# Kernel tuning notes

Measured on AMD Instinct MI355X. Metric: run time of the kernel, lower is better.

The kernel has to match this reference:

```python
import jax, jax.numpy as jnp
import numpy as np

N = 100000
E = 1600000
IN_CH = 128
HID = 32
HEADS = 4
OUT_CH = 32
NEG_SLOPE = 0.2


def _gat_layer(x, W, a_src, a_dst, b, src, dst, heads, out_ch):
    """PyG-style GATConv (concat=True). x: [N, F_in]; returns [N, heads*out_ch]."""
    n = x.shape[0]
    h = (x @ W).reshape(n, heads, out_ch)                    # [N, H, C]
    alpha_s = jnp.einsum('nhc,hc->nh', h, a_src)             # [N, H]
    alpha_d = jnp.einsum('nhc,hc->nh', h, a_dst)             # [N, H]
    logits = jax.nn.leaky_relu(alpha_s[src] + alpha_d[dst], NEG_SLOPE)  # [E, H]
    # segment softmax over destination node
    m = jax.ops.segment_max(logits, dst, num_segments=n)
    m = jnp.where(jnp.isfinite(m), m, 0.0)
    p = jnp.exp(logits - m[dst])
    denom = jax.ops.segment_sum(p, dst, num_segments=n)
    alpha = p / (denom[dst] + 1e-16)                         # [E, H]
    msg = h[src] * alpha[..., None]                          # [E, H, C]
    out = jax.ops.segment_sum(msg, dst, num_segments=n)      # [N, H, C]
    return out.reshape(n, heads * out_ch) + b


def setup_inputs() -> dict:
    key = jax.random.key(0)
    ks = jax.random.split(key, 16)
    x = jax.random.normal(ks[0], (N, IN_CH), dtype=jnp.float32)
    edge_index = jax.random.randint(ks[1], (2, E), 0, N, dtype=jnp.int32)

    def glorot(k, shape):
        fan = shape[0] + shape[-1]
        return jax.random.normal(k, shape, dtype=jnp.float32) * np.sqrt(2.0 / fan)

    hid = HID * HEADS  # 128
    return {
        'x': x,
        'edge_index': edge_index,
        'W1': glorot(ks[2], (IN_CH, hid)),
        'a_src1': glorot(ks[3], (HEADS, HID)),
        'a_dst1': glorot(ks[4], (HEADS, HID)),
        'b1': jnp.zeros((hid,), jnp.float32),
        'W2': glorot(ks[5], (hid, hid)),
        'a_src2': glorot(ks[6], (HEADS, HID)),
        'a_dst2': glorot(ks[7], (HEADS, HID)),
        'b2': jnp.zeros((hid,), jnp.float32),
        'W3': glorot(ks[8], (hid, OUT_CH)),
        'a_src3': glorot(ks[9], (1, OUT_CH)),
        'a_dst3': glorot(ks[10], (1, OUT_CH)),
        'b3': jnp.zeros((OUT_CH,), jnp.float32),
    }


def reference(x, edge_index, W1, a_src1, a_dst1, b1, W2, a_src2, a_dst2, b2,
              W3, a_src3, a_dst3, b3):
    # add self-loops (PyG GATConv default add_self_loops=True)
    loop = jnp.arange(N, dtype=edge_index.dtype)
    src = jnp.concatenate([edge_index[0], loop])
    dst = jnp.concatenate([edge_index[1], loop])

    h = _gat_layer(x, W1, a_src1, a_dst1, b1, src, dst, HEADS, HID)
    h = jax.nn.elu(h)
    h = _gat_layer(h, W2, a_src2, a_dst2, b2, src, dst, HEADS, HID)
    h = jax.nn.elu(h)
    out = _gat_layer(h, W3, a_src3, a_dst3, b3, src, dst, 1, OUT_CH)
    return out
```

## Files before the change

kernel.cpp:

```cpp
#include <hip/hip_runtime.h>
#include <cstdint>

#define NN 100000
#define EE 1600000
#define ET (EE + NN)
#define NBUCK 782
#define BCAP 3584
#define G_GEMM 1563
#define G_FILL 256
#define G_WPREP 80

typedef unsigned int u32;
typedef unsigned short u16;
typedef short bf16x8 __attribute__((ext_vector_type(8)));
typedef float f32x4 __attribute__((ext_vector_type(4)));

__device__ __forceinline__ u16 f2bf(float f) {
    union { float f; u32 i; } v; v.f = f;
    u32 r = v.i + 0x7FFFu + ((v.i >> 16) & 1u);
    return (u16)(r >> 16);
}
__device__ __forceinline__ float bf_lo(u32 u) {
    union { u32 i; float f; } v; v.i = u << 16; return v.f;
}
__device__ __forceinline__ float bf_hi(u32 u) {
    union { u32 i; float f; } v; v.i = u & 0xffff0000u; return v.f;
}
__device__ __forceinline__ void get_edge(const int* __restrict__ ei, int e, int& s, int& d) {
    if (e < EE) { s = ei[e]; d = ei[EE + e]; }
    else { s = e - EE; d = s; }
}
__device__ __forceinline__ float leaky(float x) { return x > 0.f ? x : 0.2f * x; }

template<int OUTC, bool IN16, bool WCVT>
__device__ __forceinline__ void gemm_body(int r0, u32* lds,
    const void* __restrict__ Xv, const void* __restrict__ Wsrc,
    const float* __restrict__ asw, const float* __restrict__ adw,
    u16* __restrict__ Hout16, float* __restrict__ as_o, float* __restrict__ ad_o, int tid)
{
    constexpr int NT = OUTC / 16;
    constexpr int HS = (OUTC == 128) ? 132 : 36;
    u32* wl = lds + 64 * 68;

    if (IN16) {
        const u32* Xg = (const u32*)Xv;
        for (int i = tid; i < 64 * 64; i += 256) {
            int r = i >> 6, k2 = i & 63;
            u32 v = 0;
            if (r0 + r < NN) v = Xg[(size_t)(r0 + r) * 64 + k2];
            lds[r * 68 + k2] = v;
        }
    } else {
        const float* Xf = (const float*)Xv;
        for (int i = tid; i < 64 * 64; i += 256) {
            int r = i >> 6, k2 = i & 63;
            u32 v = 0;
            if (r0 + r < NN) {
                float2 f = *(const float2*)(Xf + (size_t)(r0 + r) * 128 + k2 * 2);
                v = (u32)f2bf(f.x) | ((u32)f2bf(f.y) << 16);
            }
            lds[r * 68 + k2] = v;
        }
    }
    if (WCVT) {
        const float* Wf = (const float*)Wsrc;
        for (int i = tid; i < 128 * 64; i += 256) {
            int c = i & 127, k2 = i >> 7;
            float f0 = Wf[(2 * k2) * 128 + c];
            float f1 = Wf[(2 * k2 + 1) * 128 + c];
            wl[c * 68 + k2] = (u32)f2bf(f0) | ((u32)f2bf(f1) << 16);
        }
    } else {
        const u32* Wg = (const u32*)Wsrc;
        for (int i = tid; i < OUTC * 64; i += 256) {
            int c = i >> 6, k2 = i & 63;
            wl[c * 68 + k2] = Wg[i];
        }
    }
    __syncthreads();

    const int w = tid >> 6, l = tid & 63;
    const int lm = l & 15, q = l >> 4;

    f32x4 acc[NT];
    #pragma unroll
    for (int T = 0; T < NT; T++)
        #pragma unroll
        for (int r = 0; r < 4; r++) acc[T][r] = 0.f;

    #pragma unroll
    for (int kc = 0; kc < 4; kc++) {
        bf16x8 af = *(const bf16x8*)&lds[(16 * w + lm) * 68 + kc * 16 + q * 4];
        #pragma unroll
        for (int T = 0; T < NT; T++) {
            bf16x8 bfr = *(const bf16x8*)&wl[(16 * T + lm) * 68 + kc * 16 + q * 4];
            acc[T] = __builtin_amdgcn_mfma_f32_16x16x32_bf16(af, bfr, acc[T], 0, 0, 0);
        }
    }
    __syncthreads();

    float* hl = (float*)lds;
    #pragma unroll
    for (int T = 0; T < NT; T++)
        #pragma unroll
        for (int rg = 0; rg < 4; rg++)
            hl[(16 * w + q * 4 + rg) * HS + 16 * T + lm] = acc[T][rg];
    __syncthreads();

    for (int i = tid; i < 64 * (OUTC / 2); i += 256) {
        int r = i / (OUTC / 2), k2 = i % (OUTC / 2);
        int row = r0 + r;
        if (row < NN) {
            float a = hl[r * HS + k2 * 2];
            float b = hl[r * HS + k2 * 2 + 1];
            ((u32*)Hout16)[(size_t)row * (OUTC / 2) + k2] = (u32)f2bf(a) | ((u32)f2bf(b) << 16);
        }
    }
    if (OUTC == 128) {
        const int row = tid >> 2, part = tid & 3;
        const float* hp = &hl[row * HS + part * 32];
        const float* aw = asw + part * 32;
        const float* dw = adw + part * 32;
        float s = 0.f, d = 0.f;
        #pragma unroll
        for (int c = 0; c < 32; c++) { float hv = hp[c]; s += hv * aw[c]; d += hv * dw[c]; }
        const int grow = r0 + row;
        if (grow < NN) { as_o[(size_t)grow * 4 + part] = s; ad_o[(size_t)grow * 4 + part] = d; }
    } else {
        if (tid < 64) {
            const float* hp = &hl[tid * HS];
            float s = 0.f, d = 0.f;
            #pragma unroll
            for (int c = 0; c < 32; c++) { float hv = hp[c]; s += hv * asw[c]; d += hv * adw[c]; }
            const int grow = r0 + tid;
            if (grow < NN) { as_o[grow] = s; ad_o[grow] = d; }
        }
    }
}

__device__ __forceinline__ void bin_fill_body(int bid, int* hist, int* base,
    const int* __restrict__ ei, int* __restrict__ gcur, u32* __restrict__ pairs, int t)
{
    for (int i = t; i < NBUCK; i += 256) hist[i] = 0;
    __syncthreads();
    const int chunk = (ET + G_FILL - 1) / G_FILL;
    const int e0 = bid * chunk;
    const int e1 = min(e0 + chunk, ET);
    for (int e = e0 + t; e < e1; e += 256) {
        int s, d; get_edge(ei, e, s, d);
        atomicAdd(&hist[d >> 7], 1);
    }
    __syncthreads();
    for (int i = t; i < NBUCK; i += 256) {
        int c = hist[i];
        base[i] = c ? atomicAdd(&gcur[i], c) : 0;
        hist[i] = 0;
    }
    __syncthreads();
    for (int e = e0 + t; e < e1; e += 256) {
        int s, d; get_edge(ei, e, s, d);
        int b = d >> 7;
        int pos = atomicAdd(&hist[b], 1);
        pairs[(size_t)b * BCAP + base[b] + pos] = ((u32)(d & 127) << 25) | (u32)s;
    }
}

__global__ __launch_bounds__(256) void fused1_kernel(
    const float* __restrict__ X, const float* __restrict__ W1,
    const float* __restrict__ as1, const float* __restrict__ ad1,
    u16* __restrict__ hb16, float* __restrict__ asb, float* __restrict__ adb,
    const int* __restrict__ ei, int* __restrict__ gcur, u32* __restrict__ pairs,
    const float* __restrict__ W2, const float* __restrict__ W3,
    u16* __restrict__ wt2, u16* __restrict__ wt3)
{
    __shared__ __align__(16) u32 smem[13056];
    const int bid = blockIdx.x;
    const int tid = threadIdx.x;
    if (bid < G_GEMM) {
        gemm_body<128, false, true>(bid * 64, smem, X, W1, as1, ad1, hb16, asb, adb, tid);
    } else if (bid < G_GEMM + G_FILL) {
        int* hist = (int*)smem;
        bin_fill_body(bid - G_GEMM, hist, hist + NBUCK, ei, gcur, pairs, tid);
    } else {
        int i = (bid - G_GEMM - G_FILL) * 256 + tid;
        if (i < 16384)      { int c = i >> 7, k = i & 127; wt2[i] = f2bf(W2[k * 128 + c]); }
        else                { int j = i - 16384; int c = j >> 7, k = j & 127; wt3[j] = f2bf(W3[k * 32 + c]); }
    }
}

template<int OUTC>
__global__ __launch_bounds__(256) void gemm_mfma(
    const void* __restrict__ Xv, const u16* __restrict__ Wt16g,
    const float* __restrict__ asw, const float* __restrict__ adw,
    u16* __restrict__ Hout16, float* __restrict__ as_o, float* __restrict__ ad_o)
{
    constexpr int LDSU = (OUTC == 128) ? 13056 : 6528;
    __shared__ __align__(16) u32 lds[LDSU];
    gemm_body<OUTC, true, false>(blockIdx.x * 64, lds, Xv, Wt16g, asw, adw,
                                 Hout16, as_o, ad_o, threadIdx.x);
}

__global__ __launch_bounds__(1024) void bscan_kernel(const int* __restrict__ bcnt,
    int* __restrict__ bbase, int* __restrict__ rowp)
{
    __shared__ int lds[1024];
    const int t = threadIdx.x;
    int v = (t < NBUCK) ? bcnt[t] : 0;
    lds[t] = v;
    __syncthreads();
    for (int off = 1; off < 1024; off <<= 1) {
        int x = (t >= off) ? lds[t - off] : 0;
        __syncthreads();
        lds[t] += x;
        __syncthreads();
    }
    if (t < NBUCK) bbase[t] = lds[t] - v;
    if (t == 0) { bbase[NBUCK] = ET; rowp[NN] = ET; }
}

__global__ __launch_bounds__(256) void bucket_csr_kernel(const u32* __restrict__ pairs,
    const int* __restrict__ bcnt, const int* __restrict__ bbase,
    int* __restrict__ rowp, int* __restrict__ col)
{
    __shared__ int hist[128], scn[128];
    __shared__ int col_lds[BCAP];
    const int b = blockIdx.x;
    const int cbase = bbase[b];
    const int cnt = bcnt[b];
    const u32* pk0 = pairs + (size_t)b * BCAP;
    const int t = threadIdx.x;
    if (t < 128) hist[t] = 0;
    __syncthreads();
    for (int i = t; i < cnt; i += 256)
        atomicAdd(&hist[pk0[i] >> 25], 1);
    __syncthreads();
    if (t < 128) scn[t] = hist[t];
    __syncthreads();
    for (int off = 1; off < 128; off <<= 1) {
        int x = (t < 128 && t >= off) ? scn[t - off] : 0;
        __syncthreads();
        if (t < 128) scn[t] += x;
        __syncthreads();
    }
    if (t < 128) {
        int ex = scn[t] - hist[t];
        int node = b * 128 + t;
        if (node < NN) rowp[node] = cbase + ex;
        hist[t] = ex;
    }
    __syncthreads();
    for (int i = t; i < cnt; i += 256) {
        u32 pk = pk0[i];
        int pos = atomicAdd(&hist[pk >> 25], 1);
        if (pos < BCAP) col_lds[pos] = pk & 0x1FFFFFFu;
    }
    __syncthreads();
    for (int i = t; i < cnt; i += 256)
        col[cbase + i] = col_lds[i];
}

template<bool DOELU>
__global__ __launch_bounds__(256) void agg4g_kernel(
    const int* __restrict__ rowp, const int* __restrict__ col,
    const float* __restrict__ as_, const float* __restrict__ ad_,
    const u16* __restrict__ Hb16, const float* __restrict__ bias,
    u16* __restrict__ outp16)
{
    __shared__ float pex[4 * 288];
    __shared__ u32   sex[4 * 64];
    const int tid = threadIdx.x;
    const int wv = tid >> 6;
    const int lane = tid & 63;
    const int g = lane >> 4;
    const int sub = lane & 15;
    const int H = sub >> 2;
    const int node = blockIdx.x * 16 + wv * 4 + g;

    const int start = rowp[node];
    const int end   = rowp[node + 1];
    const float4 ad4 = ((const float4*)ad_)[node];
    const float4* as4 = (const float4*)as_;
    float* pb = &pex[wv * 288 + g * 68];
    u32*   sb = &sex[wv * 64 + g * 16];
    const char* hbase = (const char*)Hb16 + sub * 16;

    float m0 = -1e30f, m1 = -1e30f, m2 = -1e30f, m3 = -1e30f;
    float d0 = 0.f, d1 = 0.f, d2 = 0.f, d3 = 0.f;
    float a[8];
    #pragma unroll
    for (int i = 0; i < 8; i++) a[i] = 0.f;

    for (int j0 = start; j0 < end; j0 += 16) {
        const int j = j0 + sub;
        const bool valid = (j < end);
        const int s = valid ? col[j] : 0;
        const float4 av = as4[s];
        float l0 = valid ? leaky(av.x + ad4.x) : -1e30f;
        float l1 = valid ? leaky(av.y + ad4.y) : -1e30f;
        float l2 = valid ? leaky(av.z + ad4.z) : -1e30f;
        float l3 = valid ? leaky(av.w + ad4.w) : -1e30f;
        float c0 = l0, c1 = l1, c2 = l2, c3 = l3;
        #pragma unroll
        for (int off = 8; off; off >>= 1) {
            c0 = fmaxf(c0, __shfl_xor(c0, off, 16));
            c1 = fmaxf(c1, __shfl_xor(c1, off, 16));
            c2 = fmaxf(c2, __shfl_xor(c2, off, 16));
            c3 = fmaxf(c3, __shfl_xor(c3, off, 16));
        }
        const float n0 = fmaxf(m0, c0), n1 = fmaxf(m1, c1);
        const float n2 = fmaxf(m2, c2), n3 = fmaxf(m3, c3);
        const float s0 = __expf(m0 - n0), s1 = __expf(m1 - n1);
        const float s2 = __expf(m2 - n2), s3 = __expf(m3 - n3);
        float p0 = valid ? __expf(l0 - n0) : 0.f;
        float p1 = valid ? __expf(l1 - n1) : 0.f;
        float p2 = valid ? __expf(l2 - n2) : 0.f;
        float p3 = valid ? __expf(l3 - n3) : 0.f;
        float q0 = p0, q1 = p1, q2 = p2, q3 = p3;
        #pragma unroll
        for (int off = 8; off; off >>= 1) {
            q0 += __shfl_xor(q0, off, 16);
            q1 += __shfl_xor(q1, off, 16);
            q2 += __shfl_xor(q2, off, 16);
            q3 += __shfl_xor(q3, off, 16);
        }
        d0 = d0 * s0 + q0; d1 = d1 * s1 + q1;
        d2 = d2 * s2 + q2; d3 = d3 * s3 + q3;
        m0 = n0; m1 = n1; m2 = n2; m3 = n3;
        const float scH = (H == 0) ? s0 : (H == 1) ? s1 : (H == 2) ? s2 : s3;
        #pragma unroll
        for (int i = 0; i < 8; i++) a[i] *= scH;
        pb[sub * 4 + 0] = p0; pb[sub * 4 + 1] = p1;
        pb[sub * 4 + 2] = p2; pb[sub * 4 + 3] = p3;
        sb[sub] = (u32)s << 8;
        u32 so[16]; float pi[16];
        #pragma unroll
        for (int i = 0; i < 16; i++) { so[i] = sb[i]; pi[i] = pb[i * 4 + H]; }
        #pragma unroll
        for (int i = 0; i < 16; i++) {
            const uint4 w = *(const uint4*)(hbase + so[i]);
            a[0] += pi[i] * bf_lo(w.x); a[1] += pi[i] * bf_hi(w.x);
            a[2] += pi[i] * bf_lo(w.y); a[3] += pi[i] * bf_hi(w.y);
            a[4] += pi[i] * bf_lo(w.z); a[5] += pi[i] * bf_hi(w.z);
            a[6] += pi[i] * bf_lo(w.w); a[7] += pi[i] * bf_hi(w.w);
        }
    }
    const float denH = (H == 0) ? d0 : (H == 1) ? d1 : (H == 2) ? d2 : d3;
    const float r = 1.f / (denH + 1e-16f);
    const float4 b0 = ((const float4*)bias)[sub * 2];
    const float4 b1 = ((const float4*)bias)[sub * 2 + 1];
    float v[8];
    v[0] = a[0] * r + b0.x; v[1] = a[1] * r + b0.y;
    v[2] = a[2] * r + b0.z; v[3] = a[3] * r + b0.w;
    v[4] = a[4] * r + b1.x; v[5] = a[5] * r + b1.y;
    v[6] = a[6] * r + b1.z; v[7] = a[7] * r + b1.w;
    if (DOELU) {
        #pragma unroll
        for (int i = 0; i < 8; i++) v[i] = v[i] > 0.f ? v[i] : (__expf(v[i]) - 1.f);
    }
    uint4 o;
    o.x = (u32)f2bf(v[0]) | ((u32)f2bf(v[1]) << 16);
    o.y = (u32)f2bf(v[2]) | ((u32)f2bf(v[3]) << 16);
    o.z = (u32)f2bf(v[4]) | ((u32)f2bf(v[5]) << 16);
    o.w = (u32)f2bf(v[6]) | ((u32)f2bf(v[7]) << 16);
    *(uint4*)(outp16 + (size_t)node * 128 + sub * 8) = o;
}

__global__ __launch_bounds__(256) void agg1_kernel(
    const int* __restrict__ rowp, const int* __restrict__ col,
    const float* __restrict__ as_, const float* __restrict__ ad_,
    const u16* __restrict__ Hb16, const float* __restrict__ bias,
    float* __restrict__ outp)
{
    const int t = threadIdx.x;
    const int lane = t & 31;
    const int node = blockIdx.x * 8 + (t >> 5);

    const int start = rowp[node];
    const int end   = rowp[node + 1];
    const float adv = ad_[node];
    const char* hbase = (const char*)Hb16 + lane * 2;
    const float bvv = bias[lane];

    float m = -1e30f, den = 0.f, acc = 0.f;
    for (int j0 = start; j0 < end; j0 += 32) {
        const int j = j0 + lane;
        const bool valid = (j < end);
        const int s = valid ? col[j] : 0;
        const float lg = valid ? leaky(as_[s] + adv) : -1e30f;
        float cm = lg;
        #pragma unroll
        for (int off = 16; off; off >>= 1) cm = fmaxf(cm, __shfl_xor(cm, off, 32));
        const float mnew = fmaxf(m, cm);
        const float sc = __expf(m - mnew);
        acc *= sc; den *= sc; m = mnew;
        const float p = valid ? __expf(lg - m) : 0.f;
        float ps = p;
        #pragma unroll
        for (int off = 16; off; off >>= 1) ps += __shfl_xor(ps, off, 32);
        den += ps;
        const int soff = s << 6;
        int so[32]; float pi[32];
        #pragma unroll
        for (int i = 0; i < 32; i++) {
            so[i] = __shfl(soff, i, 32);
            pi[i] = __shfl(p, i, 32);
        }
        #pragma unroll
        for (int i = 0; i < 32; i++)
            acc += pi[i] * bf_lo((u32)*(const u16*)(hbase + so[i]));
    }
    outp[(size_t)node * 32 + lane] = acc / (den + 1e-16f) + bvv;
}

extern "C" void kernel_launch(void* const* d_in, const int* in_sizes, int n_in,
                              void* d_out, int out_size, void* d_ws, size_t ws_size,
                              hipStream_t stream)
{
    const float* x   = (const float*)d_in[0];
    const int*   ei  = (const int*)d_in[1];
    const float* W1  = (const float*)d_in[2];
    const float* as1 = (const float*)d_in[3];
    const float* ad1 = (const float*)d_in[4];
    const float* b1  = (const float*)d_in[5];
    const float* W2  = (const float*)d_in[6];
    const float* as2 = (const float*)d_in[7];
    const float* ad2 = (const float*)d_in[8];
    const float* b2  = (const float*)d_in[9];
    const float* W3  = (const float*)d_in[10];
    const float* as3 = (const float*)d_in[11];
    const float* ad3 = (const float*)d_in[12];
    const float* b3  = (const float*)d_in[13];
    float* outp = (float*)d_out;

    char* ws = (char*)d_ws;
    u16*   hb16  = (u16*)(ws);
    u16*   xb16  = (u16*)(ws + 25700000);
    u16*   h3b16 = (u16*)(ws + 51400000);
    float* asb   = (float*)(ws + 57900000);
    float* adb   = (float*)(ws + 59500000);
    int*   rowp  = (int*)(ws + 61100000);
    int*   col   = (int*)(ws + 61600000);
    u32*   pairs = (u32*)(ws + 68400032);
    int*   gcur  = (int*)(ws + 79700000);
    int*   bbase = (int*)(ws + 79704096);
    u16*   wt2   = (u16*)(ws + 79750000);
    u16*   wt3   = (u16*)(ws + 79790000);

    const dim3 B(256);
    const int gG = (NN + 63) / 64;

    hipMemsetAsync(gcur, 0, NBUCK * 4, stream);
    fused1_kernel<<<G_GEMM + G_FILL + G_WPREP, B, 0, stream>>>(
        x, W1, as1, ad1, hb16, asb, adb, ei, gcur, pairs, W2, W3, wt2, wt3);
    bscan_kernel<<<1, dim3(1024), 0, stream>>>(gcur, bbase, rowp);
    bucket_csr_kernel<<<NBUCK, B, 0, stream>>>(pairs, gcur, bbase, rowp, col);

    agg4g_kernel<true><<<NN / 16, B, 0, stream>>>(rowp, col, asb, adb, hb16, b1, xb16);

    gemm_mfma<128><<<gG, B, 0, stream>>>(xb16, wt2, as2, ad2, hb16, asb, adb);
    agg4g_kernel<true><<<NN / 16, B, 0, stream>>>(rowp, col, asb, adb, hb16, b2, xb16);

    gemm_mfma<32><<<gG, B, 0, stream>>>(xb16, wt3, as3, ad3, h3b16, asb, adb);
    agg1_kernel<<<NN / 8, B, 0, stream>>>(rowp, col, asb, adb, h3b16, b3, outp);
}
```

Baseline: 475.6 us.

## Unfuse first-layer kernel, pretransform W1 once, prefetch next edge chunk in aggregation

```diff
diff --git a/kernel.cpp b/kernel.cpp
--- a/kernel.cpp
+++ b/kernel.cpp
@@ -6,9 +6,7 @@
 #define ET (EE + NN)
 #define NBUCK 782
 #define BCAP 3584
-#define G_GEMM 1563
-#define G_FILL 256
-#define G_WPREP 80
+#define G_FILL 128
 
 typedef unsigned int u32;
 typedef unsigned short u16;
@@ -32,15 +30,30 @@
 }
 __device__ __forceinline__ float leaky(float x) { return x > 0.f ? x : 0.2f * x; }
 
-template<int OUTC, bool IN16, bool WCVT>
-__device__ __forceinline__ void gemm_body(int r0, u32* lds,
-    const void* __restrict__ Xv, const void* __restrict__ Wsrc,
+__global__ __launch_bounds__(256) void wprep_kernel(
+    const float* __restrict__ W1, const float* __restrict__ W2, const float* __restrict__ W3,
+    u16* __restrict__ wt1, u16* __restrict__ wt2, u16* __restrict__ wt3)
+{
+    int i = blockIdx.x * 256 + threadIdx.x;
+    if (i < 16384)      { int c = i >> 7, k = i & 127; wt1[i] = f2bf(W1[k * 128 + c]); }
+    else if (i < 32768) { int j = i - 16384; int c = j >> 7, k = j & 127; wt2[j] = f2bf(W2[k * 128 + c]); }
+    else if (i < 36864) { int j = i - 32768; int c = j >> 7, k = j & 127; wt3[j] = f2bf(W3[k * 32 + c]); }
+}
+
+template<int OUTC, bool IN16>
+__global__ __launch_bounds__(256) void gemm_mfma(
+    const void* __restrict__ Xv, const u16* __restrict__ Wt16g,
     const float* __restrict__ asw, const float* __restrict__ adw,
-    u16* __restrict__ Hout16, float* __restrict__ as_o, float* __restrict__ ad_o, int tid)
+    u16* __restrict__ Hout16, float* __restrict__ as_o, float* __restrict__ ad_o)
 {
     constexpr int NT = OUTC / 16;
+    constexpr int LDSU = (OUTC == 128) ? 13056 : 6528;
     constexpr int HS = (OUTC == 128) ? 132 : 36;
+    __shared__ __align__(16) u32 lds[LDSU];
     u32* wl = lds + 64 * 68;
+
+    const int tid = threadIdx.x;
+    const int r0 = blockIdx.x * 64;
 
     if (IN16) {
         const u32* Xg = (const u32*)Xv;
@@ -62,16 +75,8 @@
             lds[r * 68 + k2] = v;
         }
     }
-    if (WCVT) {
-        const float* Wf = (const float*)Wsrc;
-        for (int i = tid; i < 128 * 64; i += 256) {
-            int c = i & 127, k2 = i >> 7;
-            float f0 = Wf[(2 * k2) * 128 + c];
-            float f1 = Wf[(2 * k2 + 1) * 128 + c];
-            wl[c * 68 + k2] = (u32)f2bf(f0) | ((u32)f2bf(f1) << 16);
-        }
-    } else {
-        const u32* Wg = (const u32*)Wsrc;
+    {
+        const u32* Wg = (const u32*)Wt16g;
         for (int i = tid; i < OUTC * 64; i += 256) {
             int c = i >> 6, k2 = i & 63;
             wl[c * 68 + k2] = Wg[i];
@@ -138,13 +143,16 @@
     }
 }
 
-__device__ __forceinline__ void bin_fill_body(int bid, int* hist, int* base,
-    const int* __restrict__ ei, int* __restrict__ gcur, u32* __restrict__ pairs, int t)
-{
+__global__ __launch_bounds__(256) void bin_fill_kernel(const int* __restrict__ ei,
+    int* __restrict__ gcur, u32* __restrict__ pairs)
+{
+    __shared__ int hist[NBUCK];
+    __shared__ int base[NBUCK];
+    const int t = threadIdx.x;
     for (int i = t; i < NBUCK; i += 256) hist[i] = 0;
     __syncthreads();
     const int chunk = (ET + G_FILL - 1) / G_FILL;
-    const int e0 = bid * chunk;
+    const int e0 = blockIdx.x * chunk;
     const int e1 = min(e0 + chunk, ET);
     for (int e = e0 + t; e < e1; e += 256) {
         int s, d; get_edge(ei, e, s, d);
@@ -163,41 +171,6 @@
         int pos = atomicAdd(&hist[b], 1);
         pairs[(size_t)b * BCAP + base[b] + pos] = ((u32)(d & 127) << 25) | (u32)s;
     }
-}
-
-__global__ __launch_bounds__(256) void fused1_kernel(
-    const float* __restrict__ X, const float* __restrict__ W1,
-    const float* __restrict__ as1, const float* __restrict__ ad1,
-    u16* __restrict__ hb16, float* __restrict__ asb, float* __restrict__ adb,
-    const int* __restrict__ ei, int* __restrict__ gcur, u32* __restrict__ pairs,
-    const float* __restrict__ W2, const float* __restrict__ W3,
-    u16* __restrict__ wt2, u16* __restrict__ wt3)
-{
-    __shared__ __align__(16) u32 smem[13056];
-    const int bid = blockIdx.x;
-    const int tid = threadIdx.x;
-    if (bid < G_GEMM) {
-        gemm_body<128, false, true>(bid * 64, smem, X, W1, as1, ad1, hb16, asb, adb, tid);
-    } else if (bid < G_GEMM + G_FILL) {
-        int* hist = (int*)smem;
-        bin_fill_body(bid - G_GEMM, hist, hist + NBUCK, ei, gcur, pairs, tid);
-    } else {
-        int i = (bid - G_GEMM - G_FILL) * 256 + tid;
-        if (i < 16384)      { int c = i >> 7, k = i & 127; wt2[i] = f2bf(W2[k * 128 + c]); }
-        else                { int j = i - 16384; int c = j >> 7, k = j & 127; wt3[j] = f2bf(W3[k * 32 + c]); }
-    }
-}
-
-template<int OUTC>
-__global__ __launch_bounds__(256) void gemm_mfma(
-    const void* __restrict__ Xv, const u16* __restrict__ Wt16g,
-    const float* __restrict__ asw, const float* __restrict__ adw,
-    u16* __restrict__ Hout16, float* __restrict__ as_o, float* __restrict__ ad_o)
-{
-    constexpr int LDSU = (OUTC == 128) ? 13056 : 6528;
-    __shared__ __align__(16) u32 lds[LDSU];
-    gemm_body<OUTC, true, false>(blockIdx.x * 64, lds, Xv, Wt16g, asw, adw,
-                                 Hout16, as_o, ad_o, threadIdx.x);
 }
 
 __global__ __launch_bounds__(1024) void bscan_kernel(const int* __restrict__ bcnt,
@@ -290,11 +263,16 @@
     #pragma unroll
     for (int i = 0; i < 8; i++) a[i] = 0.f;
 
+    bool valid = (start + sub) < end;
+    int s = valid ? col[start + sub] : 0;
+    float4 av = as4[s];
+
     for (int j0 = start; j0 < end; j0 += 16) {
-        const int j = j0 + sub;
-        const bool valid = (j < end);
-        const int s = valid ? col[j] : 0;
-        const float4 av = as4[s];
+        const int jn = j0 + 16 + sub;
+        const bool vnext = (jn < end);
+        const int snext = vnext ? col[jn] : 0;
+        const float4 avn = as4[snext];
+
         float l0 = valid ? leaky(av.x + ad4.x) : -1e30f;
         float l1 = valid ? leaky(av.y + ad4.y) : -1e30f;
         float l2 = valid ? leaky(av.z + ad4.z) : -1e30f;
@@ -343,6 +321,7 @@
             a[4] += pi[i] * bf_lo(w.z); a[5] += pi[i] * bf_hi(w.z);
             a[6] += pi[i] * bf_lo(w.w); a[7] += pi[i] * bf_hi(w.w);
         }
+        s = snext; av = avn; valid = vnext;
     }
     const float denH = (H == 0) ? d0 : (H == 1) ? d1 : (H == 2) ? d2 : d3;
     const float r = 1.f / (denH + 1e-16f);
@@ -382,11 +361,17 @@
     const float bvv = bias[lane];
 
     float m = -1e30f, den = 0.f, acc = 0.f;
+    bool valid = (start + lane) < end;
+    int s = valid ? col[start + lane] : 0;
+    float asv = as_[s];
+
     for (int j0 = start; j0 < end; j0 += 32) {
-        const int j = j0 + lane;
-        const bool valid = (j < end);
-        const int s = valid ? col[j] : 0;
-        const float lg = valid ? leaky(as_[s] + adv) : -1e30f;
+        const int jn = j0 + 32 + lane;
+        const bool vnext = (jn < end);
+        const int snext = vnext ? col[jn] : 0;
+        const float asn = as_[snext];
+
+        const float lg = valid ? leaky(asv + adv) : -1e30f;
         float cm = lg;
         #pragma unroll
         for (int off = 16; off; off >>= 1) cm = fmaxf(cm, __shfl_xor(cm, off, 32));
@@ -408,6 +393,7 @@
         #pragma unroll
         for (int i = 0; i < 32; i++)
             acc += pi[i] * bf_lo((u32)*(const u16*)(hbase + so[i]));
+        s = snext; asv = asn; valid = vnext;
     }
     outp[(size_t)node * 32 + lane] = acc / (den + 1e-16f) + bvv;
 }
@@ -443,23 +429,25 @@
     u32*   pairs = (u32*)(ws + 68400032);
     int*   gcur  = (int*)(ws + 79700000);
     int*   bbase = (int*)(ws + 79704096);
+    u16*   wt1   = (u16*)(ws + 79710000);
     u16*   wt2   = (u16*)(ws + 79750000);
     u16*   wt3   = (u16*)(ws + 79790000);
 
     const dim3 B(256);
     const int gG = (NN + 63) / 64;
 
+    wprep_kernel<<<144, B, 0, stream>>>(W1, W2, W3, wt1, wt2, wt3);
     hipMemsetAsync(gcur, 0, NBUCK * 4, stream);
-    fused1_kernel<<<G_GEMM + G_FILL + G_WPREP, B, 0, stream>>>(
-        x, W1, as1, ad1, hb16, asb, adb, ei, gcur, pairs, W2, W3, wt2, wt3);
+    bin_fill_kernel<<<G_FILL, B, 0, stream>>>(ei, gcur, pairs);
     bscan_kernel<<<1, dim3(1024), 0, stream>>>(gcur, bbase, rowp);
     bucket_csr_kernel<<<NBUCK, B, 0, stream>>>(pairs, gcur, bbase, rowp, col);
 
+    gemm_mfma<128, false><<<gG, B, 0, stream>>>(x, wt1, as1, ad1, hb16, asb, adb);
     agg4g_kernel<true><<<NN / 16, B, 0, stream>>>(rowp, col, asb, adb, hb16, b1, xb16);
 
-    gemm_mfma<128><<<gG, B, 0, stream>>>(xb16, wt2, as2, ad2, hb16, asb, adb);
+    gemm_mfma<128, true><<<gG, B, 0, stream>>>(xb16, wt2, as2, ad2, hb16, asb, adb);
     agg4g_kernel<true><<<NN / 16, B, 0, stream>>>(rowp, col, asb, adb, hb16, b2, xb16);
 
-    gemm_mfma<32><<<gG, B, 0, stream>>>(xb16, wt3, as3, ad3, h3b16, asb, adb);
+    gemm_mfma<32, true><<<gG, B, 0, stream>>>(xb16, wt3, as3, ad3, h3b16, asb, adb);
     agg1_kernel<<<NN / 8, B, 0, stream>>>(rowp, col, asb, adb, h3b16, b3, outp);
 }
```

Result: faster. 462.6 us (-2.7%).
